# Performance work log

Hardware: AMD Instinct MI355X
Metric: run time of the kernel (lower is better)

The kernel has to match this reference:

```python
import jax, jax.numpy as jnp
import numpy as np

B, L, E, H, M = 4, 4096, 512, 8, 128
DH = E // H  # 64


def _create_projection_matrix(m, d, seed=42):
    # Faithful to torch create_projection_matrix (scaling=False): stacked QR blocks
    # scaled row-wise by norms of a gaussian matrix.
    rng = np.random.RandomState(seed)
    blocks = []
    for _ in range(m // d):
        q, _ = np.linalg.qr(rng.randn(d, d))
        blocks.append(q.T)
    rem = m - (m // d) * d
    if rem > 0:
        q, _ = np.linalg.qr(rng.randn(d, d))
        blocks.append(q.T[:rem])
    mat = np.vstack(blocks)  # [m, d]
    mult = np.linalg.norm(rng.randn(m, d), axis=1)  # [m]
    return jnp.asarray(mult[:, None] * mat, dtype=jnp.float32)


def setup_inputs() -> dict:
    key = jax.random.key(0)
    ks = jax.random.split(key, 8)
    a = float(np.sqrt(6.0 / (E + E)))  # xavier_uniform bound
    inp = {
        "query": jax.random.normal(ks[0], (B, L, E), jnp.float32),
        "key": jax.random.normal(ks[1], (B, L, E), jnp.float32),
        "value": jax.random.normal(ks[2], (B, L, E), jnp.float32),
        "Wq": jax.random.uniform(ks[3], (E, E), jnp.float32, -a, a),
        "Wk": jax.random.uniform(ks[4], (E, E), jnp.float32, -a, a),
        "Wv": jax.random.uniform(ks[5], (E, E), jnp.float32, -a, a),
        "W0": jax.random.normal(ks[6], (E, E), jnp.float32),  # W0 not xavier'd in source
        "bq": jnp.zeros((E,), jnp.float32),
        "bk": jnp.zeros((E,), jnp.float32),
        "bv": jnp.zeros((E,), jnp.float32),
        "b0": jnp.zeros((E,), jnp.float32),
        "proj": _create_projection_matrix(M, DH),
    }
    return inp


def _softmax_kernel(data, proj, is_query, eps=1e-5):
    # data: [B, L, H, DH], proj: [M, DH]
    dn = float(data.shape[-1]) ** -0.25
    ratio = float(proj.shape[0]) ** -0.5
    d_ = dn * data
    dash = jnp.einsum("blhd,md->blhm", d_, proj)  # [B,L,H,M]
    diag = 0.5 * jnp.sum(d_ * d_, axis=-1, keepdims=True)  # [B,L,H,1]
    mx = jnp.max(dash, axis=-1, keepdims=True)  # [B,L,H,1]
    if not is_query:
        mx = jnp.max(mx, axis=-3, keepdims=True)  # global over L for keys
    return ratio * (jnp.exp(dash - diag - mx) + eps)


def _causal_favor(qp, kp, v):
    # qp, kp: [L,B,H,M]; v: [L,B,H,DH]
    def step(carry, xs):
        kv_sum, k_sum = carry
        q, k, vv = xs
        kv_sum = kv_sum + k[..., :, None] * vv[..., None, :]  # [B,H,M,DH]
        k_sum = k_sum + k  # [B,H,M]
        num = jnp.einsum("bhmd,bhm->bhd", kv_sum, q)
        den = jnp.einsum("bhm,bhm->bh", q, k_sum)
        return (kv_sum, k_sum), (num, den)

    init = (
        jnp.zeros((qp.shape[1], qp.shape[2], qp.shape[3], v.shape[-1]), qp.dtype),
        jnp.zeros((qp.shape[1], qp.shape[2], qp.shape[3]), qp.dtype),
    )
    _, (num, den) = jax.lax.scan(step, init, (qp, kp, v))
    return num / den[..., None]  # [L,B,H,DH]


def reference(query, key, value, Wq, Wk, Wv, W0, bq, bk, bv, b0, proj):
    q = query @ Wq.T + bq
    k = key @ Wk.T + bk
    v = value @ Wv.T + bv
    q = q.reshape(B, L, H, DH)
    k = k.reshape(B, L, H, DH)
    v = v.reshape(B, L, H, DH)

    qp = _softmax_kernel(q, proj, True)   # [B,L,H,M]
    kp = _softmax_kernel(k, proj, False)  # [B,L,H,M]

    # move L to front for the causal scan
    out = _causal_favor(
        jnp.moveaxis(qp, 1, 0), jnp.moveaxis(kp, 1, 0), jnp.moveaxis(v, 1, 0)
    )  # [L,B,H,DH]
    out = jnp.moveaxis(out, 0, 1).reshape(B, L, E)
    return out @ W0.T + b0
```

## Files before the change

### kernel.cpp

```cpp
#include <hip/hip_runtime.h>
#include <math.h>


typedef unsigned short u16;
typedef short s8v __attribute__((ext_vector_type(8)));
typedef unsigned short u4v __attribute__((ext_vector_type(4)));
typedef float f4v __attribute__((ext_vector_type(4)));

#define DN_    0.35355339059327379f
#define RATIO_ 0.08838834764831845f
#define EPS_   1e-5f

static __device__ __forceinline__ u16 f2bf(float x) {
  union { float f; unsigned u; } v; v.f = x;
  unsigned r = v.u + 0x7fffu + ((v.u >> 16) & 1u);
  return (u16)(r >> 16);
}
static __device__ __forceinline__ float bf2f(u16 b) {
  union { unsigned u; float f; } v; v.u = ((unsigned)b) << 16;
  return v.f;
}
static __device__ __forceinline__ unsigned fmax_key(float f) {
  union { float f; unsigned u; } v; v.f = f;
  return (v.u & 0x80000000u) ? ~v.u : (v.u | 0x80000000u);
}
static __device__ __forceinline__ float fmax_unkey(unsigned k) {
  union { unsigned u; float f; } v;
  v.u = (k & 0x80000000u) ? (k ^ 0x80000000u) : ~k;
  return v.f;
}
static __device__ __forceinline__ f4v mfma16(s8v a, s8v b, f4v c) {
  return __builtin_amdgcn_mfma_f32_16x16x32_bf16(a, b, c, 0, 0, 0);
}
static __device__ __forceinline__ void bar_lds() {
  asm volatile("s_waitcnt lgkmcnt(0)" ::: "memory");
  __builtin_amdgcn_s_barrier();
}
static __device__ __forceinline__ s8v pack8(f4v a, f4v b) {
  union { s8v v; unsigned u[4]; } r;
  asm("v_cvt_pk_bf16_f32 %0, %1, %2" : "=v"(r.u[0]) : "v"(a[0]), "v"(a[1]));
  asm("v_cvt_pk_bf16_f32 %0, %1, %2" : "=v"(r.u[1]) : "v"(a[2]), "v"(a[3]));
  asm("v_cvt_pk_bf16_f32 %0, %1, %2" : "=v"(r.u[2]) : "v"(b[0]), "v"(b[1]));
  asm("v_cvt_pk_bf16_f32 %0, %1, %2" : "=v"(r.u[3]) : "v"(b[2]), "v"(b[3]));
  return r.v;
}
static __device__ __forceinline__ int sw(int row, int col, int ldc) {
  int c3 = col >> 3;
  c3 = (c3 & ~7) | ((c3 ^ row) & 7);
  return row * ldc + (c3 << 3) + (col & 7);
}

__global__ __launch_bounds__(256) void convw_k(
    const float* __restrict__ Wq, const float* __restrict__ Wk,
    const float* __restrict__ Wv, const float* __restrict__ W0,
    const float* __restrict__ proj, u16* __restrict__ out) {
  const int i = blockIdx.x * 256 + threadIdx.x;
  const float* s;
  float scale = 1.f;
  if (i < 131072) {
    const int zz = i >> 15;
    s = (zz == 0 ? Wq : zz == 1 ? Wk : zz == 2 ? Wv : W0) + (size_t)(i & 32767) * 8;
  } else {
    s = proj + (size_t)(i - 131072) * 8;
    scale = DN_;
  }
  f4v a = *(const f4v*)s, b = *(const f4v*)(s + 4);
#pragma unroll
  for (int j = 0; j < 4; j++) { a[j] *= scale; b[j] *= scale; }
  *(s8v*)(out + (size_t)i * 8) = pack8(a, b);
}

__global__ __launch_bounds__(256) void gemm3_k(
    const float* __restrict__ Aq, const float* __restrict__ Ak, const float* __restrict__ Av,
    const u16* __restrict__ Wb,
    const float* __restrict__ bq, const float* __restrict__ bk, const float* __restrict__ bv,
    u16* __restrict__ Cq, u16* __restrict__ Ck, u16* __restrict__ vT) {
  const int z = blockIdx.z;
  const float* Ap = (z == 0) ? Aq : (z == 1) ? Ak : Av;
  const u16* Bm = Wb + (size_t)z * 262144;
  const float* bias = (z == 0) ? bq : (z == 1) ? bk : bv;

  __shared__ u16 LB[2][8192];
  u16* const Al = LB[0];
  u16* const Bl = LB[1];
  const int tid = threadIdx.x;
  const int r0 = blockIdx.x * 128, c0 = blockIdx.y * 128;
  const int lane = tid & 63, w = tid >> 6;
  const int l15 = lane & 15, l4 = lane >> 4;
  const int wr = (w >> 1) * 64, wc = (w & 1) * 64;
  const f4v z4 = {0.f, 0.f, 0.f, 0.f};
  f4v acc[4][4];
#pragma unroll
  for (int m = 0; m < 4; m++)
#pragma unroll
    for (int n = 0; n < 4; n++) acc[m][n] = z4;

  f4v pa0_0, pa0_1, pa1_0, pa1_1, pa2_0, pa2_1, pa3_0, pa3_1;
  s8v pb0, pb1, pb2, pb3;

#define LOADT(kt)                                                             \
  {                                                                           \
    const int u0 = tid, u1 = tid + 256, u2 = tid + 512, u3 = tid + 768;       \
    const float* s0 = Ap + (size_t)(r0 + (u0 >> 3)) * 512 + (kt) + ((u0 & 7) << 3); \
    const float* s1 = Ap + (size_t)(r0 + (u1 >> 3)) * 512 + (kt) + ((u1 & 7) << 3); \
    const float* s2 = Ap + (size_t)(r0 + (u2 >> 3)) * 512 + (kt) + ((u2 & 7) << 3); \
    const float* s3 = Ap + (size_t)(r0 + (u3 >> 3)) * 512 + (kt) + ((u3 & 7) << 3); \
    pa0_0 = *(const f4v*)s0; pa0_1 = *(const f4v*)(s0 + 4);                   \
    pa1_0 = *(const f4v*)s1; pa1_1 = *(const f4v*)(s1 + 4);                   \
    pa2_0 = *(const f4v*)s2; pa2_1 = *(const f4v*)(s2 + 4);                   \
    pa3_0 = *(const f4v*)s3; pa3_1 = *(const f4v*)(s3 + 4);                   \
    pb0 = *(const s8v*)(Bm + (size_t)(c0 + (u0 >> 3)) * 512 + (kt) + ((u0 & 7) << 3)); \
    pb1 = *(const s8v*)(Bm + (size_t)(c0 + (u1 >> 3)) * 512 + (kt) + ((u1 & 7) << 3)); \
    pb2 = *(const s8v*)(Bm + (size_t)(c0 + (u2 >> 3)) * 512 + (kt) + ((u2 & 7) << 3)); \
    pb3 = *(const s8v*)(Bm + (size_t)(c0 + (u3 >> 3)) * 512 + (kt) + ((u3 & 7) << 3)); \
  }
#define WRITET()                                                              \
  {                                                                           \
    const int u0 = tid, u1 = tid + 256, u2 = tid + 512, u3 = tid + 768;       \
    const int d0 = sw(u0 >> 3, (u0 & 7) << 3, 64);                            \
    const int d1 = sw(u1 >> 3, (u1 & 7) << 3, 64);                            \
    const int d2 = sw(u2 >> 3, (u2 & 7) << 3, 64);                            \
    const int d3 = sw(u3 >> 3, (u3 & 7) << 3, 64);                            \
    *(s8v*)&Al[d0] = pack8(pa0_0, pa0_1); *(s8v*)&Bl[d0] = pb0;               \
    *(s8v*)&Al[d1] = pack8(pa1_0, pa1_1); *(s8v*)&Bl[d1] = pb1;               \
    *(s8v*)&Al[d2] = pack8(pa2_0, pa2_1); *(s8v*)&Bl[d2] = pb2;               \
    *(s8v*)&Al[d3] = pack8(pa3_0, pa3_1); *(s8v*)&Bl[d3] = pb3;               \
  }

  LOADT(0);
  WRITET();
  bar_lds();

  for (int t = 0; t < 8; t++) {
    if (t < 7) LOADT((t + 1) * 64);
#pragma unroll
    for (int ks = 0; ks < 2; ks++) {
      s8v af[4], bf[4];
#pragma unroll
      for (int m = 0; m < 4; m++)
        af[m] = *(const s8v*)&Al[sw(wr + m * 16 + l15, ks * 32 + l4 * 8, 64)];
#pragma unroll
      for (int n = 0; n < 4; n++)
        bf[n] = *(const s8v*)&Bl[sw(wc + n * 16 + l15, ks * 32 + l4 * 8, 64)];
#pragma unroll
      for (int m = 0; m < 4; m++)
#pragma unroll
        for (int n = 0; n < 4; n++) acc[m][n] = mfma16(af[m], bf[n], acc[m][n]);
    }
    bar_lds();
    if (t < 7) {
      WRITET();
      bar_lds();
    }
  }
#undef LOADT
#undef WRITET

  if (z == 2) {
    u16* const T = &LB[0][0];
#pragma unroll
    for (int n = 0; n < 4; n++) {
      const int cc = wc + n * 16 + l15;
      const float bv_ = bias[c0 + cc];
#pragma unroll
      for (int m = 0; m < 4; m++)
#pragma unroll
        for (int r = 0; r < 4; r++) {
          const int ll = wr + m * 16 + l4 * 4 + r;
          const int ch = ll >> 3;
          const int chs = (ch & 8) | ((ch ^ cc) & 7);
          T[cc * 128 + chs * 8 + (ll & 7)] = f2bf(acc[m][n][r] + bv_);
        }
    }
    __syncthreads();
    const int b = r0 >> 12, l0 = r0 & 4095;
    for (int u = tid; u < 2048; u += 256) {
      const int cc = u >> 4, ch = u & 15;
      const int chs = (ch & 8) | ((ch ^ cc) & 7);
      const s8v o = *(const s8v*)&T[cc * 128 + chs * 8];
      *(s8v*)(vT + ((size_t)(b * 512 + c0 + cc)) * 4096 + l0 + ch * 8) = o;
    }
    return;
  }
  u16* const Cp = (z == 0) ? Cq : Ck;
#pragma unroll
  for (int n = 0; n < 4; n++) {
    const int col = c0 + wc + n * 16 + l15;
    const float bv_ = bias[col];
#pragma unroll
    for (int m = 0; m < 4; m++)
#pragma unroll
      for (int r = 0; r < 4; r++) {
        const int row = r0 + wr + m * 16 + l4 * 4 + r;
        Cp[(size_t)row * 512 + col] = f2bf(acc[m][n][r] + bv_);
      }
  }
}

__global__ __launch_bounds__(256) void gemm_bt(const u16* __restrict__ Ap,
                                               const u16* __restrict__ Bm,
                                               const float* __restrict__ bias,
                                               float* __restrict__ Cp) {
  __shared__ u16 Al[128 * 64];
  __shared__ u16 Bl[128 * 64];
  const int tid = threadIdx.x;
  const int r0 = blockIdx.x * 128, c0 = blockIdx.y * 128;
  const int lane = tid & 63, w = tid >> 6;
  const int l15 = lane & 15, l4 = lane >> 4;
  const int wr = (w >> 1) * 64, wc = (w & 1) * 64;
  const f4v z = {0.f, 0.f, 0.f, 0.f};
  f4v acc[4][4];
#pragma unroll
  for (int m = 0; m < 4; m++)
#pragma unroll
    for (int n = 0; n < 4; n++) acc[m][n] = z;

  s8v qa0, qa1, qa2, qa3, qb0, qb1, qb2, qb3;
#define LOADT(kt)                                                             \
  {                                                                           \
    const int u0 = tid, u1 = tid + 256, u2 = tid + 512, u3 = tid + 768;       \
    qa0 = *(const s8v*)(Ap + (size_t)(r0 + (u0 >> 3)) * 512 + (kt) + ((u0 & 7) << 3)); \
    qa1 = *(const s8v*)(Ap + (size_t)(r0 + (u1 >> 3)) * 512 + (kt) + ((u1 & 7) << 3)); \
    qa2 = *(const s8v*)(Ap + (size_t)(r0 + (u2 >> 3)) * 512 + (kt) + ((u2 & 7) << 3)); \
    qa3 = *(const s8v*)(Ap + (size_t)(r0 + (u3 >> 3)) * 512 + (kt) + ((u3 & 7) << 3)); \
    qb0 = *(const s8v*)(Bm + (size_t)(c0 + (u0 >> 3)) * 512 + (kt) + ((u0 & 7) << 3)); \
    qb1 = *(const s8v*)(Bm + (size_t)(c0 + (u1 >> 3)) * 512 + (kt) + ((u1 & 7) << 3)); \
    qb2 = *(const s8v*)(Bm + (size_t)(c0 + (u2 >> 3)) * 512 + (kt) + ((u2 & 7) << 3)); \
    qb3 = *(const s8v*)(Bm + (size_t)(c0 + (u3 >> 3)) * 512 + (kt) + ((u3 & 7) << 3)); \
  }
#define WRITET()                                                              \
  {                                                                           \
    const int u0 = tid, u1 = tid + 256, u2 = tid + 512, u3 = tid + 768;       \
    const int d0 = sw(u0 >> 3, (u0 & 7) << 3, 64);                            \
    const int d1 = sw(u1 >> 3, (u1 & 7) << 3, 64);                            \
    const int d2 = sw(u2 >> 3, (u2 & 7) << 3, 64);                            \
    const int d3 = sw(u3 >> 3, (u3 & 7) << 3, 64);                            \
    *(s8v*)&Al[d0] = qa0; *(s8v*)&Bl[d0] = qb0;                               \
    *(s8v*)&Al[d1] = qa1; *(s8v*)&Bl[d1] = qb1;                               \
    *(s8v*)&Al[d2] = qa2; *(s8v*)&Bl[d2] = qb2;                               \
    *(s8v*)&Al[d3] = qa3; *(s8v*)&Bl[d3] = qb3;                               \
  }

  LOADT(0);
  WRITET();
  bar_lds();

  for (int t = 0; t < 8; t++) {
    if (t < 7) LOADT((t + 1) * 64);
#pragma unroll
    for (int ks = 0; ks < 2; ks++) {
      s8v af[4], bf[4];
#pragma unroll
      for (int m = 0; m < 4; m++)
        af[m] = *(const s8v*)&Al[sw(wr + m * 16 + l15, ks * 32 + l4 * 8, 64)];
#pragma unroll
      for (int n = 0; n < 4; n++)
        bf[n] = *(const s8v*)&Bl[sw(wc + n * 16 + l15, ks * 32 + l4 * 8, 64)];
#pragma unroll
      for (int m = 0; m < 4; m++)
#pragma unroll
        for (int n = 0; n < 4; n++) acc[m][n] = mfma16(af[m], bf[n], acc[m][n]);
    }
    bar_lds();
    if (t < 7) {
      WRITET();
      bar_lds();
    }
  }
#undef LOADT
#undef WRITET

#pragma unroll
  for (int n = 0; n < 4; n++) {
    const int col = c0 + wc + n * 16 + l15;
    const float bv = bias[col];
#pragma unroll
    for (int m = 0; m < 4; m++)
#pragma unroll
      for (int r = 0; r < 4; r++) {
        const int row = r0 + wr + m * 16 + l4 * 4 + r;
        Cp[(size_t)row * 512 + col] = acc[m][n][r] + bv;
      }
  }
}

template<int MODE>
__global__ __launch_bounds__(256) void feat_kernel(const u16* __restrict__ X,
                                                   const u16* __restrict__ pDN,
                                                   u16* __restrict__ outp,
                                                   unsigned* __restrict__ slots) {
  __shared__ u16 Xl[128 * 64];
  __shared__ u16 Pl[128 * 64];
  __shared__ float diag_l[128];
  __shared__ unsigned hmax8[8];
  const int tid = threadIdx.x;
  const int r0 = blockIdx.x * 128;
  if (MODE == 1 && tid < 8) hmax8[tid] = 0u;
  for (int u = tid; u < 1024; u += 256) {
    const int row = u >> 3, c8 = (u & 7) << 3;
    *(s8v*)&Xl[sw(row, c8, 64)] = *(const s8v*)(X + (size_t)r0 * 64 + u * 8);
    *(s8v*)&Pl[sw(row, c8, 64)] = *(const s8v*)(pDN + u * 8);
  }
  __syncthreads();
  if (MODE == 0 && tid < 128) {
    float s = 0.f;
#pragma unroll
    for (int c = 0; c < 8; c++) {
      s8v v = *(const s8v*)&Xl[sw(tid, c * 8, 64)];
#pragma unroll
      for (int jj = 0; jj < 8; jj++) { float x = bf2f((u16)v[jj]); s += x * x; }
    }
    diag_l[tid] = 0.0625f * s;
  }
  __syncthreads();
  const int lane = tid & 63, w = tid >> 6, l15 = lane & 15, l4 = lane >> 4;
  const f4v z = {0.f, 0.f, 0.f, 0.f};
  f4v acc[2][8];
#pragma unroll
  for (int m = 0; m < 2; m++)
#pragma unroll
    for (int n = 0; n < 8; n++) acc[m][n] = z;
#pragma unroll
  for (int ks = 0; ks < 2; ks++) {
    s8v af[2];
#pragma unroll
    for (int m = 0; m < 2; m++)
      af[m] = *(const s8v*)&Xl[sw(w * 32 + m * 16 + l15, ks * 32 + l4 * 8, 64)];
#pragma unroll
    for (int n = 0; n < 8; n++) {
      const s8v bf = *(const s8v*)&Pl[sw(n * 16 + l15, ks * 32 + l4 * 8, 64)];
#pragma unroll
      for (int m = 0; m < 2; m++) acc[m][n] = mfma16(af[m], bf, acc[m][n]);
    }
  }
#pragma unroll
  for (int m = 0; m < 2; m++)
#pragma unroll
    for (int r = 0; r < 4; r++) {
      const int rowl = w * 32 + m * 16 + l4 * 4 + r;
      const int R = r0 + rowl;
      float mx = acc[m][0][r];
#pragma unroll
      for (int n = 1; n < 8; n++) mx = fmaxf(mx, acc[m][n][r]);
      mx = fmaxf(mx, __shfl_xor(mx, 1, 64));
      mx = fmaxf(mx, __shfl_xor(mx, 2, 64));
      mx = fmaxf(mx, __shfl_xor(mx, 4, 64));
      mx = fmaxf(mx, __shfl_xor(mx, 8, 64));
      if (MODE == 1) {
        if (l15 == 0) atomicMax(&hmax8[(l4 * 4 + r) & 7], fmax_key(mx));
      } else {
        const float sub = diag_l[rowl] + mx;
        const size_t ob = (size_t)R * 128 + l15;
#pragma unroll
        for (int n = 0; n < 8; n++)
          outp[ob + n * 16] = f2bf(RATIO_ * (expf(acc[m][n][r] - sub) + EPS_));
      }
    }
  if (MODE == 1) {
    __syncthreads();
    if (tid < 8) atomicMax(&slots[((r0 >> 15) << 3) | tid], hmax8[tid]);
  }
}

__global__ __launch_bounds__(256) void feat2h_k(const u16* __restrict__ k_b,
                                                const u16* __restrict__ pDN,
                                                u16* __restrict__ kp,
                                                u16* __restrict__ kpT,
                                                const unsigned* __restrict__ slots) {
  __shared__ u16 S[16384];
  __shared__ float diag_l[128];
  u16* const Xl = S;
  u16* const Pl = S + 8192;
  const int lt = blockIdx.x, bh = blockIdx.y;
  const int b = bh >> 3, h = bh & 7;
  const int l0 = lt * 128;
  const int tid = threadIdx.x;
  for (int u = tid; u < 1024; u += 256) {
    const int row = u >> 3, c8 = (u & 7) << 3;
    *(s8v*)&Xl[sw(row, c8, 64)] =
        *(const s8v*)(k_b + ((size_t)(b * 4096 + l0 + row)) * 512 + h * 64 + c8);
    *(s8v*)&Pl[sw(row, c8, 64)] = *(const s8v*)(pDN + u * 8);
  }
  __syncthreads();
  if (tid < 128) {
    float s = 0.f;
#pragma unroll
    for (int c = 0; c < 8; c++) {
      s8v v = *(const s8v*)&Xl[sw(tid, c * 8, 64)];
#pragma unroll
      for (int jj = 0; jj < 8; jj++) { float x = bf2f((u16)v[jj]); s += x * x; }
    }
    diag_l[tid] = 0.0625f * s;
  }
  __syncthreads();
  const int lane = tid & 63, w = tid >> 6, l15 = lane & 15, l4 = lane >> 4;
  const f4v z = {0.f, 0.f, 0.f, 0.f};
  f4v acc[2][8];
#pragma unroll
  for (int m = 0; m < 2; m++)
#pragma unroll
    for (int n = 0; n < 8; n++) acc[m][n] = z;
#pragma unroll
  for (int ks = 0; ks < 2; ks++) {
    s8v af[2];
#pragma unroll
    for (int m = 0; m < 2; m++)
      af[m] = *(const s8v*)&Xl[sw(w * 32 + m * 16 + l15, ks * 32 + l4 * 8, 64)];
#pragma unroll
    for (int n = 0; n < 8; n++) {
      const s8v bf = *(const s8v*)&Pl[sw(n * 16 + l15, ks * 32 + l4 * 8, 64)];
#pragma unroll
      for (int m = 0; m < 2; m++) acc[m][n] = mfma16(af[m], bf, acc[m][n]);
    }
  }
  const float gmax = fmax_unkey(slots[bh]);
  __syncthreads();
#pragma unroll
  for (int mm = 0; mm < 2; mm++)
#pragma unroll
    for (int r = 0; r < 4; r++) {
      const int ll = w * 32 + mm * 16 + l4 * 4 + r;
      const float sub = diag_l[ll] + gmax;
      const size_t ob = ((size_t)(b * 4096 + l0 + ll) * 8 + h) * 128 + l15;
      const int ch = ll >> 3;
#pragma unroll
      for (int n = 0; n < 8; n++) {
        const u16 val = f2bf(RATIO_ * (expf(acc[mm][n][r] - sub) + EPS_));
        kp[ob + n * 16] = val;
        const int m = n * 16 + l15;
        const int chs = (ch & 8) | ((ch ^ m) & 7);
        S[m * 128 + chs * 8 + (ll & 7)] = val;
      }
    }
  __syncthreads();
  for (int u = tid; u < 2048; u += 256) {
    const int m = u >> 4, ch = u & 15;
    const int chs = (ch & 8) | ((ch ^ m) & 7);
    const s8v o = *(const s8v*)&S[m * 128 + chs * 8];
    *(s8v*)(kpT + ((size_t)(bh * 128 + m)) * 4096 + l0 + ch * 8) = o;
  }
}

__global__ __launch_bounds__(256) void scan1_k(const u16* __restrict__ vT,
                                               const u16* __restrict__ kpT,
                                               u16* __restrict__ st,
                                               float* __restrict__ colsum) {
  __shared__ u16 Vl[64 * 128];
  __shared__ u16 Kl[128 * 128];
  const int c = blockIdx.x, bh = blockIdx.y;
  const int tid = threadIdx.x, lane = tid & 63, w = tid >> 6;
  const int l15 = lane & 15, l4 = lane >> 4;
  for (int u = tid; u < 1024; u += 256) {
    const int row = u >> 4, c8 = (u & 15) * 8;
    *(s8v*)&Vl[sw(row, c8, 128)] =
        *(const s8v*)(vT + ((size_t)(bh * 64 + row)) * 4096 + c * 128 + c8);
  }
  for (int u = tid; u < 2048; u += 256) {
    const int row = u >> 4, c8 = (u & 15) * 8;
    *(s8v*)&Kl[sw(row, c8, 128)] =
        *(const s8v*)(kpT + ((size_t)(bh * 128 + row)) * 4096 + c * 128 + c8);
  }
  __syncthreads();
  const f4v z = {0.f, 0.f, 0.f, 0.f};
  f4v acc[8];
#pragma unroll
  for (int n = 0; n < 8; n++) acc[n] = z;
#pragma unroll
  for (int ks = 0; ks < 4; ks++) {
    const s8v af = *(const s8v*)&Vl[sw(w * 16 + l15, ks * 32 + l4 * 8, 128)];
#pragma unroll
    for (int n = 0; n < 8; n++) {
      const s8v bf = *(const s8v*)&Kl[sw(n * 16 + l15, ks * 32 + l4 * 8, 128)];
      acc[n] = mfma16(af, bf, acc[n]);
    }
  }
  if (tid < 128) {
    float s = 0.f;
#pragma unroll
    for (int j8 = 0; j8 < 16; j8++) {
      s8v v = *(const s8v*)&Kl[sw(tid, j8 * 8, 128)];
#pragma unroll
      for (int jj = 0; jj < 8; jj++) s += bf2f((u16)v[jj]);
    }
    colsum[((size_t)(bh * 32 + c)) * 128 + tid] = s;
  }
  const size_t base = ((size_t)(bh * 32 + c)) * 8192;
#pragma unroll
  for (int n = 0; n < 8; n++)
#pragma unroll
    for (int r = 0; r < 4; r++)
      st[base + (w * 16 + l4 * 4 + r) * 128 + n * 16 + l15] = f2bf(acc[n][r]);
}

__global__ __launch_bounds__(256) void scan2_k(u16* __restrict__ st) {
  const int seg = blockIdx.x, bh = blockIdx.y, tid = threadIdx.x;
  const int e0 = seg * 1024 + tid * 4;
  float acc[4] = {0.f, 0.f, 0.f, 0.f};
  for (int c = 0; c < 32; c++) {
    u16* p = st + ((size_t)(bh * 32 + c)) * 8192 + e0;
    u4v v = *(u4v*)p, o;
#pragma unroll
    for (int j = 0; j < 4; j++) {
      const float x = bf2f(v[j]);
      o[j] = f2bf(acc[j]);
      acc[j] += x;
    }
    *(u4v*)p = o;
  }
}

__global__ __launch_bounds__(128) void kpref_k(const float* __restrict__ colsum,
                                               float* __restrict__ kpref) {
  const int bh = blockIdx.x, m = threadIdx.x;
  float ka = 0.f;
  for (int c = 0; c < 32; c++) {
    kpref[(bh * 32 + c) * 128 + m] = ka;
    ka += colsum[(bh * 32 + c) * 128 + m];
  }
}

__global__ __launch_bounds__(256) void scan3_k(const u16* __restrict__ qp,
                                               const u16* __restrict__ kp,
                                               const u16* __restrict__ vT,
                                               const u16* __restrict__ st,
                                               const float* __restrict__ kpref,
                                               u16* __restrict__ attn) {
  __shared__ u16 Ql[64 * 128];
  __shared__ u16 Kr[128 * 128];
  const int c = blockIdx.x, half = blockIdx.y, bh = blockIdx.z;
  const int b = bh >> 3, h = bh & 7;
  const int tid = threadIdx.x, lane = tid & 63, w = tid >> 6;
  const int l15 = lane & 15, l4 = lane >> 4;
  const size_t Rbase = ((size_t)(b * 4096 + c * 128)) * 8 + h;

  for (int u = tid; u < 1024; u += 256) {
    const int row = u >> 4, c8 = (u & 15) * 8;
    *(s8v*)&Ql[sw(row, c8, 128)] =
        *(const s8v*)(qp + (Rbase + (size_t)(half * 64 + row) * 8) * 128 + c8);
  }
  for (int u = tid; u < 2048; u += 256) {
    const int row = u >> 4, c8 = (u & 15) * 8;
    *(s8v*)&Kr[sw(row, c8, 128)] =
        *(const s8v*)(kp + (Rbase + (size_t)row * 8) * 128 + c8);
  }
  __syncthreads();

  const f4v z = {0.f, 0.f, 0.f, 0.f};
  f4v sc[8];
#pragma unroll
  for (int n = 0; n < 8; n++) sc[n] = z;
#pragma unroll
  for (int ks = 0; ks < 4; ks++) {
    const s8v af = *(const s8v*)&Ql[sw(w * 16 + l15, ks * 32 + l4 * 8, 128)];
#pragma unroll
    for (int n = 0; n < 8; n++) {
      const s8v bf = *(const s8v*)&Kr[sw(n * 16 + l15, ks * 32 + l4 * 8, 128)];
      sc[n] = mfma16(af, bf, sc[n]);
    }
  }
  const int lb = half * 64 + w * 16 + l4 * 4;
  float rs[4];
#pragma unroll
  for (int r = 0; r < 4; r++) {
    float s = 0.f;
#pragma unroll
    for (int n = 0; n < 8; n++) {
      const int col = n * 16 + l15;
      const float v = (col <= lb + r) ? sc[n][r] : 0.f;
      sc[n][r] = v;
      s += v;
    }
    s += __shfl_xor(s, 1, 64);
    s += __shfl_xor(s, 2, 64);
    s += __shfl_xor(s, 4, 64);
    s += __shfl_xor(s, 8, 64);
    rs[r] = s;
  }
  __syncthreads();

  {
    const u16* pref = st + ((size_t)(bh * 32 + c)) * 8192;
    for (int u = tid; u < 1024; u += 256) {
      const int row = u >> 4, c8 = (u & 15) * 8;
      *(s8v*)&Kr[sw(row, c8, 128)] = *(const s8v*)(pref + u * 8);
    }
    if (tid < 128) Kr[sw(64, tid, 128)] = f2bf(kpref[(bh * 32 + c) * 128 + tid]);
    for (int i = tid; i < 15 * 128; i += 256) Kr[65 * 128 + i] = 0;
  }
  __syncthreads();

  f4v acc2[5];
#pragma unroll
  for (int n = 0; n < 5; n++) acc2[n] = z;
#pragma unroll
  for (int ks = 0; ks < 4; ks++) {
    const s8v af = *(const s8v*)&Ql[sw(w * 16 + l15, ks * 32 + l4 * 8, 128)];
#pragma unroll
    for (int n = 0; n < 5; n++) {
      const s8v bf = *(const s8v*)&Kr[sw(n * 16 + l15, ks * 32 + l4 * 8, 128)];
      acc2[n] = mfma16(af, bf, acc2[n]);
    }
  }
  float din[4];
#pragma unroll
  for (int r = 0; r < 4; r++) {
    float s = acc2[4][r];
    s += __shfl_xor(s, 1, 64);
    s += __shfl_xor(s, 2, 64);
    s += __shfl_xor(s, 4, 64);
    s += __shfl_xor(s, 8, 64);
    din[r] = s;
  }
  __syncthreads();

#pragma unroll
  for (int n = 0; n < 8; n++)
#pragma unroll
    for (int r = 0; r < 4; r++)
      Kr[sw(w * 16 + l4 * 4 + r, n * 16 + l15, 128)] = f2bf(sc[n][r]);
  for (int u = tid; u < 1024; u += 256) {
    const int row = u >> 4, c8 = (u & 15) * 8;
    *(s8v*)&Kr[8192 + sw(row, c8, 128)] =
        *(const s8v*)(vT + ((size_t)(bh * 64 + row)) * 4096 + c * 128 + c8);
  }
  __syncthreads();

#pragma unroll
  for (int ks = 0; ks < 4; ks++) {
    const s8v af = *(const s8v*)&Kr[sw(w * 16 + l15, ks * 32 + l4 * 8, 128)];
#pragma unroll
    for (int n = 0; n < 4; n++) {
      const s8v bf = *(const s8v*)&Kr[8192 + sw(n * 16 + l15, ks * 32 + l4 * 8, 128)];
      acc2[n] = mfma16(af, bf, acc2[n]);
    }
  }
#pragma unroll
  for (int r = 0; r < 4; r++) {
    const float den = rs[r] + din[r];
    const int lrow = half * 64 + w * 16 + l4 * 4 + r;
    const size_t ob = ((size_t)(b * 4096 + c * 128 + lrow)) * 512 + h * 64;
#pragma unroll
    for (int n = 0; n < 4; n++)
      attn[ob + n * 16 + l15] = f2bf(acc2[n][r] / den);
  }
}

extern "C" void kernel_launch(void* const* d_in, const int* in_sizes, int n_in,
                              void* d_out, int out_size, void* d_ws, size_t ws_size,
                              hipStream_t stream) {
  const float* query = (const float*)d_in[0];
  const float* key   = (const float*)d_in[1];
  const float* value = (const float*)d_in[2];
  const float* Wq = (const float*)d_in[3];
  const float* Wk = (const float*)d_in[4];
  const float* Wv = (const float*)d_in[5];
  const float* W0 = (const float*)d_in[6];
  const float* bq = (const float*)d_in[7];
  const float* bk = (const float*)d_in[8];
  const float* bv = (const float*)d_in[9];
  const float* b0 = (const float*)d_in[10];
  const float* proj = (const float*)d_in[11];

  char* ws = (char*)d_ws;
  const size_t MB = 1u << 20;
  u16* kp   = (u16*)(ws + 0);
  u16* k_b  = (u16*)(ws + 32 * MB);
  u16* attn = (u16*)(ws + 32 * MB);
  float* colsum = (float*)(ws + 32 * MB);
  u16* qp   = (u16*)(ws + 48 * MB);
  u16* kpT  = (u16*)(ws + 80 * MB);
  u16* q_b  = (u16*)(ws + 80 * MB);
  u16* st   = (u16*)(ws + 112 * MB);
  u16* vT   = (u16*)(ws + 128 * MB);
  float* kpref    = (float*)(ws + 144 * MB);
  unsigned* slots = (unsigned*)(ws + 144 * MB + 524288);
  u16* Wb   = (u16*)(ws + 145 * MB);
  u16* pDN  = Wb + 4 * 262144;

  (void)hipMemsetAsync(slots, 0, 32 * sizeof(unsigned), stream);

  dim3 blk(256);
  convw_k<<<dim3(516), blk, 0, stream>>>(Wq, Wk, Wv, W0, proj, Wb);
  gemm3_k<<<dim3(128, 4, 3), blk, 0, stream>>>(query, key, value, Wb,
                                               bq, bk, bv, q_b, k_b, vT);
  feat_kernel<0><<<dim3(1024), blk, 0, stream>>>(q_b, pDN, qp, nullptr);
  feat_kernel<1><<<dim3(1024), blk, 0, stream>>>(k_b, pDN, nullptr, slots);
  feat2h_k<<<dim3(32, 32), blk, 0, stream>>>(k_b, pDN, kp, kpT, slots);
  scan1_k<<<dim3(32, 32), blk, 0, stream>>>(vT, kpT, st, colsum);
  scan2_k<<<dim3(8, 32), blk, 0, stream>>>(st);
  kpref_k<<<dim3(32), dim3(128), 0, stream>>>(colsum, kpref);
  scan3_k<<<dim3(32, 2, 32), blk, 0, stream>>>(qp, kp, vT, st, kpref, attn);
  gemm_bt<<<dim3(128, 4), blk, 0, stream>>>(attn, Wb + 3 * 262144, b0, (float*)d_out);
}
```

Measured before the change: 195.6 us.

## Halve GEMM column tiles and merge feature and prefix-scan launches

The projection GEMMs (gemm3_k and gemm_bt) now use 128x64 tiles instead of 128x128, which doubles the grid and cuts LDS per block to raise occupancy and spread work across more CUs. The separate query and key feature kernels are merged into one 2048-block launch, and the kpref prefix sum is folded into the scan2 kernel as an extra segment. Together these aim to reduce launch overhead and tail effects. In exchange the GEMMs reload A tiles twice as often and each wave does fewer MFMAs per LDS read.

```diff
diff --git a/kernel.cpp b/kernel.cpp
--- a/kernel.cpp
+++ b/kernel.cpp
@@ -80,23 +80,22 @@
   const u16* Bm = Wb + (size_t)z * 262144;
   const float* bias = (z == 0) ? bq : (z == 1) ? bk : bv;
 
-  __shared__ u16 LB[2][8192];
-  u16* const Al = LB[0];
-  u16* const Bl = LB[1];
+  __shared__ u16 Al[8192];
+  __shared__ u16 Bl[4096];
   const int tid = threadIdx.x;
-  const int r0 = blockIdx.x * 128, c0 = blockIdx.y * 128;
+  const int r0 = blockIdx.x * 128, c0 = blockIdx.y * 64;
   const int lane = tid & 63, w = tid >> 6;
   const int l15 = lane & 15, l4 = lane >> 4;
-  const int wr = (w >> 1) * 64, wc = (w & 1) * 64;
+  const int wr = (w >> 1) * 64, wc = (w & 1) * 32;
   const f4v z4 = {0.f, 0.f, 0.f, 0.f};
-  f4v acc[4][4];
+  f4v acc[4][2];
 #pragma unroll
   for (int m = 0; m < 4; m++)
 #pragma unroll
-    for (int n = 0; n < 4; n++) acc[m][n] = z4;
+    for (int n = 0; n < 2; n++) acc[m][n] = z4;
 
   f4v pa0_0, pa0_1, pa1_0, pa1_1, pa2_0, pa2_1, pa3_0, pa3_1;
-  s8v pb0, pb1, pb2, pb3;
+  s8v pb0, pb1;
 
 #define LOADT(kt)                                                             \
   {                                                                           \
@@ -111,20 +110,28 @@
     pa3_0 = *(const f4v*)s3; pa3_1 = *(const f4v*)(s3 + 4);                   \
     pb0 = *(const s8v*)(Bm + (size_t)(c0 + (u0 >> 3)) * 512 + (kt) + ((u0 & 7) << 3)); \
     pb1 = *(const s8v*)(Bm + (size_t)(c0 + (u1 >> 3)) * 512 + (kt) + ((u1 & 7) << 3)); \
-    pb2 = *(const s8v*)(Bm + (size_t)(c0 + (u2 >> 3)) * 512 + (kt) + ((u2 & 7) << 3)); \
-    pb3 = *(const s8v*)(Bm + (size_t)(c0 + (u3 >> 3)) * 512 + (kt) + ((u3 & 7) << 3)); \
   }
 #define WRITET()                                                              \
   {                                                                           \
     const int u0 = tid, u1 = tid + 256, u2 = tid + 512, u3 = tid + 768;       \
-    const int d0 = sw(u0 >> 3, (u0 & 7) << 3, 64);                            \
-    const int d1 = sw(u1 >> 3, (u1 & 7) << 3, 64);                            \
-    const int d2 = sw(u2 >> 3, (u2 & 7) << 3, 64);                            \
-    const int d3 = sw(u3 >> 3, (u3 & 7) << 3, 64);                            \
-    *(s8v*)&Al[d0] = pack8(pa0_0, pa0_1); *(s8v*)&Bl[d0] = pb0;               \
-    *(s8v*)&Al[d1] = pack8(pa1_0, pa1_1); *(s8v*)&Bl[d1] = pb1;               \
-    *(s8v*)&Al[d2] = pack8(pa2_0, pa2_1); *(s8v*)&Bl[d2] = pb2;               \
-    *(s8v*)&Al[d3] = pack8(pa3_0, pa3_1); *(s8v*)&Bl[d3] = pb3;               \
+    *(s8v*)&Al[sw(u0 >> 3, (u0 & 7) << 3, 64)] = pack8(pa0_0, pa0_1);         \
+    *(s8v*)&Al[sw(u1 >> 3, (u1 & 7) << 3, 64)] = pack8(pa1_0, pa1_1);         \
+    *(s8v*)&Al[sw(u2 >> 3, (u2 & 7) << 3, 64)] = pack8(pa2_0, pa2_1);         \
+    *(s8v*)&Al[sw(u3 >> 3, (u3 & 7) << 3, 64)] = pack8(pa3_0, pa3_1);         \
+    *(s8v*)&Bl[sw(u0 >> 3, (u0 & 7) << 3, 64)] = pb0;                         \
+    *(s8v*)&Bl[sw((u1 - 256) >> 3 | 32, (u1 & 7) << 3, 64)] = pb1;            \
+  }
+
+#undef WRITET
+#define WRITET()                                                              \
+  {                                                                           \
+    const int u0 = tid, u1 = tid + 256, u2 = tid + 512, u3 = tid + 768;       \
+    *(s8v*)&Al[sw(u0 >> 3, (u0 & 7) << 3, 64)] = pack8(pa0_0, pa0_1);         \
+    *(s8v*)&Al[sw(u1 >> 3, (u1 & 7) << 3, 64)] = pack8(pa1_0, pa1_1);         \
+    *(s8v*)&Al[sw(u2 >> 3, (u2 & 7) << 3, 64)] = pack8(pa2_0, pa2_1);         \
+    *(s8v*)&Al[sw(u3 >> 3, (u3 & 7) << 3, 64)] = pack8(pa3_0, pa3_1);         \
+    *(s8v*)&Bl[sw(u0 >> 3, (u0 & 7) << 3, 64)] = pb0;                         \
+    *(s8v*)&Bl[sw(u1 >> 3, (u1 & 7) << 3, 64)] = pb1;                         \
   }
 
   LOADT(0);
@@ -135,17 +142,17 @@
     if (t < 7) LOADT((t + 1) * 64);
 #pragma unroll
     for (int ks = 0; ks < 2; ks++) {
-      s8v af[4], bf[4];
+      s8v af[4], bf[2];
 #pragma unroll
       for (int m = 0; m < 4; m++)
         af[m] = *(const s8v*)&Al[sw(wr + m * 16 + l15, ks * 32 + l4 * 8, 64)];
 #pragma unroll
-      for (int n = 0; n < 4; n++)
+      for (int n = 0; n < 2; n++)
         bf[n] = *(const s8v*)&Bl[sw(wc + n * 16 + l15, ks * 32 + l4 * 8, 64)];
 #pragma unroll
       for (int m = 0; m < 4; m++)
 #pragma unroll
-        for (int n = 0; n < 4; n++) acc[m][n] = mfma16(af[m], bf[n], acc[m][n]);
+        for (int n = 0; n < 2; n++) acc[m][n] = mfma16(af[m], bf[n], acc[m][n]);
     }
     bar_lds();
     if (t < 7) {
@@ -157,9 +164,8 @@
 #undef WRITET
 
   if (z == 2) {
-    u16* const T = &LB[0][0];
-#pragma unroll
-    for (int n = 0; n < 4; n++) {
+#pragma unroll
+    for (int n = 0; n < 2; n++) {
       const int cc = wc + n * 16 + l15;
       const float bv_ = bias[c0 + cc];
 #pragma unroll
@@ -169,22 +175,22 @@
           const int ll = wr + m * 16 + l4 * 4 + r;
           const int ch = ll >> 3;
           const int chs = (ch & 8) | ((ch ^ cc) & 7);
-          T[cc * 128 + chs * 8 + (ll & 7)] = f2bf(acc[m][n][r] + bv_);
+          Al[cc * 128 + chs * 8 + (ll & 7)] = f2bf(acc[m][n][r] + bv_);
         }
     }
     __syncthreads();
     const int b = r0 >> 12, l0 = r0 & 4095;
-    for (int u = tid; u < 2048; u += 256) {
+    for (int u = tid; u < 1024; u += 256) {
       const int cc = u >> 4, ch = u & 15;
       const int chs = (ch & 8) | ((ch ^ cc) & 7);
-      const s8v o = *(const s8v*)&T[cc * 128 + chs * 8];
+      const s8v o = *(const s8v*)&Al[cc * 128 + chs * 8];
       *(s8v*)(vT + ((size_t)(b * 512 + c0 + cc)) * 4096 + l0 + ch * 8) = o;
     }
     return;
   }
   u16* const Cp = (z == 0) ? Cq : Ck;
 #pragma unroll
-  for (int n = 0; n < 4; n++) {
+  for (int n = 0; n < 2; n++) {
     const int col = c0 + wc + n * 16 + l15;
     const float bv_ = bias[col];
 #pragma unroll
@@ -201,21 +207,21 @@
                                                const u16* __restrict__ Bm,
                                                const float* __restrict__ bias,
                                                float* __restrict__ Cp) {
-  __shared__ u16 Al[128 * 64];
-  __shared__ u16 Bl[128 * 64];
+  __shared__ u16 Al[8192];
+  __shared__ u16 Bl[4096];
   const int tid = threadIdx.x;
-  const int r0 = blockIdx.x * 128, c0 = blockIdx.y * 128;
+  const int r0 = blockIdx.x * 128, c0 = blockIdx.y * 64;
   const int lane = tid & 63, w = tid >> 6;
   const int l15 = lane & 15, l4 = lane >> 4;
-  const int wr = (w >> 1) * 64, wc = (w & 1) * 64;
+  const int wr = (w >> 1) * 64, wc = (w & 1) * 32;
   const f4v z = {0.f, 0.f, 0.f, 0.f};
-  f4v acc[4][4];
+  f4v acc[4][2];
 #pragma unroll
   for (int m = 0; m < 4; m++)
 #pragma unroll
-    for (int n = 0; n < 4; n++) acc[m][n] = z;
-
-  s8v qa0, qa1, qa2, qa3, qb0, qb1, qb2, qb3;
+    for (int n = 0; n < 2; n++) acc[m][n] = z;
+
+  s8v qa0, qa1, qa2, qa3, qb0, qb1;
 #define LOADT(kt)                                                             \
   {                                                                           \
     const int u0 = tid, u1 = tid + 256, u2 = tid + 512, u3 = tid + 768;       \
@@ -225,20 +231,16 @@
     qa3 = *(const s8v*)(Ap + (size_t)(r0 + (u3 >> 3)) * 512 + (kt) + ((u3 & 7) << 3)); \
     qb0 = *(const s8v*)(Bm + (size_t)(c0 + (u0 >> 3)) * 512 + (kt) + ((u0 & 7) << 3)); \
     qb1 = *(const s8v*)(Bm + (size_t)(c0 + (u1 >> 3)) * 512 + (kt) + ((u1 & 7) << 3)); \
-    qb2 = *(const s8v*)(Bm + (size_t)(c0 + (u2 >> 3)) * 512 + (kt) + ((u2 & 7) << 3)); \
-    qb3 = *(const s8v*)(Bm + (size_t)(c0 + (u3 >> 3)) * 512 + (kt) + ((u3 & 7) << 3)); \
   }
 #define WRITET()                                                              \
   {                                                                           \
     const int u0 = tid, u1 = tid + 256, u2 = tid + 512, u3 = tid + 768;       \
-    const int d0 = sw(u0 >> 3, (u0 & 7) << 3, 64);                            \
-    const int d1 = sw(u1 >> 3, (u1 & 7) << 3, 64);                            \
-    const int d2 = sw(u2 >> 3, (u2 & 7) << 3, 64);                            \
-    const int d3 = sw(u3 >> 3, (u3 & 7) << 3, 64);                            \
-    *(s8v*)&Al[d0] = qa0; *(s8v*)&Bl[d0] = qb0;                               \
-    *(s8v*)&Al[d1] = qa1; *(s8v*)&Bl[d1] = qb1;                               \
-    *(s8v*)&Al[d2] = qa2; *(s8v*)&Bl[d2] = qb2;                               \
-    *(s8v*)&Al[d3] = qa3; *(s8v*)&Bl[d3] = qb3;                               \
+    *(s8v*)&Al[sw(u0 >> 3, (u0 & 7) << 3, 64)] = qa0;                         \
+    *(s8v*)&Al[sw(u1 >> 3, (u1 & 7) << 3, 64)] = qa1;                         \
+    *(s8v*)&Al[sw(u2 >> 3, (u2 & 7) << 3, 64)] = qa2;                         \
+    *(s8v*)&Al[sw(u3 >> 3, (u3 & 7) << 3, 64)] = qa3;                         \
+    *(s8v*)&Bl[sw(u0 >> 3, (u0 & 7) << 3, 64)] = qb0;                         \
+    *(s8v*)&Bl[sw(u1 >> 3, (u1 & 7) << 3, 64)] = qb1;                         \
   }
 
   LOADT(0);
@@ -249,17 +251,17 @@
     if (t < 7) LOADT((t + 1) * 64);
 #pragma unroll
     for (int ks = 0; ks < 2; ks++) {
-      s8v af[4], bf[4];
+      s8v af[4], bf[2];
 #pragma unroll
       for (int m = 0; m < 4; m++)
         af[m] = *(const s8v*)&Al[sw(wr + m * 16 + l15, ks * 32 + l4 * 8, 64)];
 #pragma unroll
-      for (int n = 0; n < 4; n++)
+      for (int n = 0; n < 2; n++)
         bf[n] = *(const s8v*)&Bl[sw(wc + n * 16 + l15, ks * 32 + l4 * 8, 64)];
 #pragma unroll
       for (int m = 0; m < 4; m++)
 #pragma unroll
-        for (int n = 0; n < 4; n++) acc[m][n] = mfma16(af[m], bf[n], acc[m][n]);
+        for (int n = 0; n < 2; n++) acc[m][n] = mfma16(af[m], bf[n], acc[m][n]);
     }
     bar_lds();
     if (t < 7) {
@@ -271,7 +273,7 @@
 #undef WRITET
 
 #pragma unroll
-  for (int n = 0; n < 4; n++) {
+  for (int n = 0; n < 2; n++) {
     const int col = c0 + wc + n * 16 + l15;
     const float bv = bias[col];
 #pragma unroll
@@ -284,25 +286,27 @@
   }
 }
 
-template<int MODE>
-__global__ __launch_bounds__(256) void feat_kernel(const u16* __restrict__ X,
-                                                   const u16* __restrict__ pDN,
-                                                   u16* __restrict__ outp,
-                                                   unsigned* __restrict__ slots) {
+__global__ __launch_bounds__(256) void feat01_k(const u16* __restrict__ q_b,
+                                                const u16* __restrict__ k_b,
+                                                const u16* __restrict__ pDN,
+                                                u16* __restrict__ qp,
+                                                unsigned* __restrict__ slots) {
   __shared__ u16 Xl[128 * 64];
   __shared__ u16 Pl[128 * 64];
   __shared__ float diag_l[128];
   __shared__ unsigned hmax8[8];
+  const int mode = blockIdx.x >> 10;
+  const int r0 = (blockIdx.x & 1023) * 128;
+  const u16* X = mode ? k_b : q_b;
   const int tid = threadIdx.x;
-  const int r0 = blockIdx.x * 128;
-  if (MODE == 1 && tid < 8) hmax8[tid] = 0u;
+  if (mode && tid < 8) hmax8[tid] = 0u;
   for (int u = tid; u < 1024; u += 256) {
     const int row = u >> 3, c8 = (u & 7) << 3;
     *(s8v*)&Xl[sw(row, c8, 64)] = *(const s8v*)(X + (size_t)r0 * 64 + u * 8);
     *(s8v*)&Pl[sw(row, c8, 64)] = *(const s8v*)(pDN + u * 8);
   }
   __syncthreads();
-  if (MODE == 0 && tid < 128) {
+  if (!mode && tid < 128) {
     float s = 0.f;
 #pragma unroll
     for (int c = 0; c < 8; c++) {
@@ -346,17 +350,17 @@
       mx = fmaxf(mx, __shfl_xor(mx, 2, 64));
       mx = fmaxf(mx, __shfl_xor(mx, 4, 64));
       mx = fmaxf(mx, __shfl_xor(mx, 8, 64));
-      if (MODE == 1) {
+      if (mode) {
         if (l15 == 0) atomicMax(&hmax8[(l4 * 4 + r) & 7], fmax_key(mx));
       } else {
         const float sub = diag_l[rowl] + mx;
         const size_t ob = (size_t)R * 128 + l15;
 #pragma unroll
         for (int n = 0; n < 8; n++)
-          outp[ob + n * 16] = f2bf(RATIO_ * (expf(acc[m][n][r] - sub) + EPS_));
+          qp[ob + n * 16] = f2bf(RATIO_ * (expf(acc[m][n][r] - sub) + EPS_));
       }
     }
-  if (MODE == 1) {
+  if (mode) {
     __syncthreads();
     if (tid < 8) atomicMax(&slots[((r0 >> 15) << 3) | tid], hmax8[tid]);
   }
@@ -492,30 +496,30 @@
       st[base + (w * 16 + l4 * 4 + r) * 128 + n * 16 + l15] = f2bf(acc[n][r]);
 }
 
-__global__ __launch_bounds__(256) void scan2_k(u16* __restrict__ st) {
+__global__ __launch_bounds__(256) void scan2p_k(u16* __restrict__ st,
+                                                const float* __restrict__ colsum,
+                                                float* __restrict__ kpref) {
   const int seg = blockIdx.x, bh = blockIdx.y, tid = threadIdx.x;
-  const int e0 = seg * 1024 + tid * 4;
-  float acc[4] = {0.f, 0.f, 0.f, 0.f};
-  for (int c = 0; c < 32; c++) {
-    u16* p = st + ((size_t)(bh * 32 + c)) * 8192 + e0;
-    u4v v = *(u4v*)p, o;
-#pragma unroll
-    for (int j = 0; j < 4; j++) {
-      const float x = bf2f(v[j]);
-      o[j] = f2bf(acc[j]);
-      acc[j] += x;
-    }
-    *(u4v*)p = o;
-  }
-}
-
-__global__ __launch_bounds__(128) void kpref_k(const float* __restrict__ colsum,
-                                               float* __restrict__ kpref) {
-  const int bh = blockIdx.x, m = threadIdx.x;
-  float ka = 0.f;
-  for (int c = 0; c < 32; c++) {
-    kpref[(bh * 32 + c) * 128 + m] = ka;
-    ka += colsum[(bh * 32 + c) * 128 + m];
+  if (seg < 8) {
+    const int e0 = seg * 1024 + tid * 4;
+    float acc[4] = {0.f, 0.f, 0.f, 0.f};
+    for (int c = 0; c < 32; c++) {
+      u16* p = st + ((size_t)(bh * 32 + c)) * 8192 + e0;
+      u4v v = *(u4v*)p, o;
+#pragma unroll
+      for (int j = 0; j < 4; j++) {
+        const float x = bf2f(v[j]);
+        o[j] = f2bf(acc[j]);
+        acc[j] += x;
+      }
+      *(u4v*)p = o;
+    }
+  } else if (tid < 128) {
+    float ka = 0.f;
+    for (int c = 0; c < 32; c++) {
+      kpref[(bh * 32 + c) * 128 + tid] = ka;
+      ka += colsum[(bh * 32 + c) * 128 + tid];
+    }
   }
 }
 
@@ -681,14 +685,12 @@
 
   dim3 blk(256);
   convw_k<<<dim3(516), blk, 0, stream>>>(Wq, Wk, Wv, W0, proj, Wb);
-  gemm3_k<<<dim3(128, 4, 3), blk, 0, stream>>>(query, key, value, Wb,
+  gemm3_k<<<dim3(128, 8, 3), blk, 0, stream>>>(query, key, value, Wb,
                                                bq, bk, bv, q_b, k_b, vT);
-  feat_kernel<0><<<dim3(1024), blk, 0, stream>>>(q_b, pDN, qp, nullptr);
-  feat_kernel<1><<<dim3(1024), blk, 0, stream>>>(k_b, pDN, nullptr, slots);
+  feat01_k<<<dim3(2048), blk, 0, stream>>>(q_b, k_b, pDN, qp, slots);
   feat2h_k<<<dim3(32, 32), blk, 0, stream>>>(k_b, pDN, kp, kpT, slots);
   scan1_k<<<dim3(32, 32), blk, 0, stream>>>(vT, kpT, st, colsum);
-  scan2_k<<<dim3(8, 32), blk, 0, stream>>>(st);
-  kpref_k<<<dim3(32), dim3(128), 0, stream>>>(colsum, kpref);
+  scan2p_k<<<dim3(9, 32), blk, 0, stream>>>(st, colsum, kpref);
   scan3_k<<<dim3(32, 2, 32), blk, 0, stream>>>(qp, kp, vT, st, kpref, attn);
-  gemm_bt<<<dim3(128, 4), blk, 0, stream>>>(attn, Wb + 3 * 262144, b0, (float*)d_out);
-}
+  gemm_bt<<<dim3(128, 8), blk, 0, stream>>>(attn, Wb + 3 * 262144, b0, (float*)d_out);
+}
```

Result: slower. 200.1 us (+2.3%).
